# Kernel optimization log

Measured on AMD Instinct MI355X. Metric: run time of the kernel, lower is better.

The kernel has to match this reference:

```python
import jax, jax.numpy as jnp
import numpy as np

ALPHA = 0.2   # leaky_relu slope inside GAT/GCN
SLOPE = 0.01  # default F.leaky_relu slope in decoder MLPs


def _leaky(x, s):
    return jnp.where(x > 0, x, s * x)


def _gat(x, mask, W, a, b):
    # AttentionLayer.forward (eval mode: attention dropout off)
    h = x @ W                                   # [N, d]
    d = W.shape[1]
    e = _leaky(h @ a[:d] + (h @ a[d:]).T, ALPHA)  # dense [N, N] scores
    att = jax.nn.softmax(jnp.where(mask > 0, e, -9e15), axis=1)
    out = _leaky(att @ h, ALPHA)
    out = out / jnp.maximum(jnp.linalg.norm(out, axis=1, keepdims=True), 1e-12)  # F.normalize p=2 dim=1
    return out + b


def reference(x, adj, gcn_W, gcn_b, hgat_W, hgat_a, hgat_b, eta,
              l1_W, l1_a, l1_b, l2_W, l2_a, l2_b, l2_rW, l2_rb,
              tf1_W, tf1_b, tf2_W, tf2_b, tg1_W, tg1_b, tg2_W, tg2_b,
              mlp_W, mlp_b, train_sample):
    N = x.shape[0]
    # normalize_adj 'sym' via row/col scaling (avoids diag matmuls)
    rowsum = adj.sum(1)
    dis = rowsum ** -0.5
    dis = jnp.where(jnp.isinf(dis), 0.0, dis)
    gcn_adj = adj * dis[:, None] * dis[None, :]
    # normalize_adj(adj,'rw') is a no-op in the source -> gat_adj = adj + I
    gat_adj = adj + jnp.eye(N, dtype=adj.dtype)

    # HybridLayer (called with gcn_adj for both branches)
    gcn_out = _leaky(gcn_adj @ (x @ gcn_W + gcn_b), 0.2)
    gat_out = _gat(x, gcn_adj, hgat_W, hgat_a, hgat_b)
    h = eta * gcn_out + (1.0 - eta) * gat_out
    h = 0.7 * h + 0.3 * jax.lax.stop_gradient(h)  # x*0.7 + x.detach()*0.3
    h = jax.nn.selu(h)

    # ConvLayer1: ResAttention heads (in==out -> identity residual), mean reduce
    h1 = jnp.mean(jnp.stack([_gat(h, gat_adj, l1_W[i], l1_a[i], l1_b[i]) + h
                             for i in range(l1_W.shape[0])]), axis=0)
    h1 = jax.nn.selu(h1)

    # ConvLayer2: ResAttention heads with linear residual projection, mean reduce
    embed = jnp.mean(jnp.stack([_gat(h1, gat_adj, l2_W[i], l2_a[i], l2_b[i])
                                + (h1 @ l2_rW[i] + l2_rb[i])
                                for i in range(l2_W.shape[0])]), axis=0)

    # decoder MLPs (eval: p=0.01 dropout omitted for determinism)
    tf = _leaky(_leaky(embed @ tf1_W + tf1_b, SLOPE) @ tf2_W + tf2_b, SLOPE)
    tg = _leaky(_leaky(embed @ tg1_W + tg1_b, SLOPE) @ tg2_W + tg2_b, SLOPE)

    pair = jnp.concatenate([tf[train_sample[:, 0]], tg[train_sample[:, 1]]], axis=1)
    return pair @ mlp_W + mlp_b  # type='MLP' decode -> [B, 2]


def setup_inputs() -> dict:
    key = jax.random.key(0)
    ks = jax.random.split(key, 32)
    N, Din, H1, H2, H3, Dout, B, NH = 6144, 512, 256, 128, 64, 32, 4096, 2
    s = 0.05
    r = lambda k, sh: (jax.random.normal(k, sh, jnp.float32) * s)
    adj = (jax.random.uniform(ks[1], (N, N)) < 0.01).astype(jnp.float32)
    return {
        'x': jax.random.normal(ks[0], (N, Din), jnp.float32),
        'adj': adj,
        'gcn_W': r(ks[2], (Din, H1)), 'gcn_b': jnp.zeros((H1,), jnp.float32),
        'hgat_W': r(ks[3], (Din, H1)), 'hgat_a': r(ks[4], (2 * H1, 1)),
        'hgat_b': jnp.zeros((H1,), jnp.float32),
        'eta': jnp.array([0.5], jnp.float32),
        'l1_W': r(ks[5], (NH, H1, H1)), 'l1_a': r(ks[6], (NH, 2 * H1, 1)),
        'l1_b': jnp.zeros((NH, H1), jnp.float32),
        'l2_W': r(ks[7], (NH, H1, H2)), 'l2_a': r(ks[8], (NH, 2 * H2, 1)),
        'l2_b': jnp.zeros((NH, H2), jnp.float32),
        'l2_rW': r(ks[9], (NH, H1, H2)), 'l2_rb': jnp.zeros((NH, H2), jnp.float32),
        'tf1_W': r(ks[10], (H2, H3)), 'tf1_b': jnp.zeros((H3,), jnp.float32),
        'tf2_W': r(ks[11], (H3, Dout)), 'tf2_b': jnp.zeros((Dout,), jnp.float32),
        'tg1_W': r(ks[12], (H2, H3)), 'tg1_b': jnp.zeros((H3,), jnp.float32),
        'tg2_W': r(ks[13], (H3, Dout)), 'tg2_b': jnp.zeros((Dout,), jnp.float32),
        'mlp_W': r(ks[14], (2 * Dout, 2)), 'mlp_b': jnp.zeros((2,), jnp.float32),
        'train_sample': jax.random.randint(ks[15], (B, 2), 0, N, jnp.int32),
    }
```

## Files before the change

### kernel.cpp

```cpp
#include <hip/hip_runtime.h>
#include <math.h>


#define NN 6144
#define CAP 256

typedef __attribute__((ext_vector_type(8))) short bf16x8;
typedef __attribute__((ext_vector_type(4))) float f32x4;

__device__ __forceinline__ unsigned short f2bf(float v) {
  unsigned u = __float_as_uint(v);
  unsigned r = u + 0x7fffu + ((u >> 16) & 1u);
  return (unsigned short)(r >> 16);
}
__device__ __forceinline__ float bf2f(unsigned short h) {
  return __uint_as_float(((unsigned)h) << 16);
}
__device__ __forceinline__ float wave_max(float v) {
#pragma unroll
  for (int off = 32; off > 0; off >>= 1) v = fmaxf(v, __shfl_xor(v, off));
  return v;
}
__device__ __forceinline__ float wave_sum(float v) {
#pragma unroll
  for (int off = 32; off > 0; off >>= 1) v += __shfl_xor(v, off);
  return v;
}
__device__ __forceinline__ float selu_f(float x) {
  const float sc = 1.0507009873554805f, al = 1.6732632423543772f;
  return x > 0.0f ? sc * x : sc * al * (__expf(x) - 1.0f);
}
__device__ __forceinline__ void write_apack4(unsigned short* __restrict__ Ah,
    unsigned short* __restrict__ Al, int KC, int m, int k0,
    float v0, float v1, float v2, float v3) {
  int mt = m >> 4, c = k0 >> 5;
  int lane = ((k0 >> 3) & 3) * 16 + (m & 15);
  int j = k0 & 7;
  size_t base = ((size_t)(mt * KC + c) * 64 + lane) * 8 + j;
  ushort4 hi, lo;
  hi.x = f2bf(v0); lo.x = f2bf(v0 - bf2f(hi.x));
  hi.y = f2bf(v1); lo.y = f2bf(v1 - bf2f(hi.y));
  hi.z = f2bf(v2); lo.z = f2bf(v2 - bf2f(hi.z));
  hi.w = f2bf(v3); lo.w = f2bf(v3 - bf2f(hi.w));
  *(ushort4*)(Ah + base) = hi;
  *(ushort4*)(Al + base) = lo;
}

__global__ __launch_bounds__(256) void build_ell(const float* __restrict__ adj,
    unsigned short* __restrict__ nbr, int* __restrict__ deg,
    int* __restrict__ selfflag, float* __restrict__ dis)
{
  __shared__ unsigned long long mS[4][6][4];
  __shared__ int cntS[4];
  __shared__ int selfS;
  int i = blockIdx.x;
  int t = threadIdx.x, lane = t & 63, w = t >> 6;
  if (t == 0) selfS = 0;
  const float* row = adj + (size_t)i * NN + w * 1536;
  int cnt = 0;
  int hasself = 0;
#pragma unroll
  for (int it = 0; it < 6; ++it) {
    float4 v = *(const float4*)(row + it * 256 + lane * 4);
    unsigned long long m0 = __ballot(v.x != 0.0f);
    unsigned long long m1 = __ballot(v.y != 0.0f);
    unsigned long long m2 = __ballot(v.z != 0.0f);
    unsigned long long m3 = __ballot(v.w != 0.0f);
    if (lane == 0) {
      mS[w][it][0] = m0; mS[w][it][1] = m1; mS[w][it][2] = m2; mS[w][it][3] = m3;
    }
    cnt += __popcll(m0) + __popcll(m1) + __popcll(m2) + __popcll(m3);
  }
  if (lane == 0) cntS[w] = cnt;
  __syncthreads();
  int base = 0;
  for (int ww = 0; ww < w; ++ww) base += cntS[ww];
  unsigned long long below = (1ull << lane) - 1ull;
#pragma unroll
  for (int it = 0; it < 6; ++it) {
    unsigned long long m0 = mS[w][it][0], m1 = mS[w][it][1];
    unsigned long long m2 = mS[w][it][2], m3 = mS[w][it][3];
    int pre = __popcll(m0 & below) + __popcll(m1 & below) +
              __popcll(m2 & below) + __popcll(m3 & below);
    int c = w * 1536 + it * 256 + lane * 4;
    int p = base + pre;
    if ((m0 >> lane) & 1) { if (p < CAP) nbr[(size_t)i * CAP + p] = (unsigned short)c;     if (c == i) hasself = 1; p++; }
    if ((m1 >> lane) & 1) { if (p < CAP) nbr[(size_t)i * CAP + p] = (unsigned short)(c+1); if (c+1 == i) hasself = 1; p++; }
    if ((m2 >> lane) & 1) { if (p < CAP) nbr[(size_t)i * CAP + p] = (unsigned short)(c+2); if (c+2 == i) hasself = 1; p++; }
    if ((m3 >> lane) & 1) { if (p < CAP) nbr[(size_t)i * CAP + p] = (unsigned short)(c+3); if (c+3 == i) hasself = 1; }
    base += __popcll(m0) + __popcll(m1) + __popcll(m2) + __popcll(m3);
  }
  if (hasself) selfS = 1;
  __syncthreads();
  if (t == 0) {
    int total = cntS[0] + cntS[1] + cntS[2] + cntS[3];
    deg[i] = total < CAP ? total : CAP;
    selfflag[i] = selfS;
    dis[i] = (total > 0) ? rsqrtf((float)total) : 0.0f;
  }
}

__global__ __launch_bounds__(256) void pack_all(const float* __restrict__ gcn_W,
    const float* __restrict__ hgat_W, const float* __restrict__ l1_W,
    const float* __restrict__ l2_W, const float* __restrict__ l2_rW,
    const float* __restrict__ x,
    unsigned short* __restrict__ Bh, unsigned short* __restrict__ Bl,
    unsigned short* __restrict__ Ah, unsigned short* __restrict__ Al,
    float* __restrict__ fgZ)
{
  int idx = blockIdx.x * 256 + threadIdx.x;
  if (idx >= 520192) return;
  if (idx >= 458752) { fgZ[idx - 458752] = 0.0f; return; }
  if (idx >= 65536) {
    int rel = idx - 65536;
    int l = rel & 63;
    int mc = rel >> 6;
    int c = mc & 15, mt = mc >> 4;
    int m = mt * 16 + (l & 15);
    int kb = c * 32 + (l >> 4) * 8;
    const float* src = x + (size_t)m * 512 + kb;
    bf16x8 vh, vl;
#pragma unroll
    for (int j = 0; j < 8; ++j) {
      float v = src[j];
      unsigned short h = f2bf(v);
      vh[j] = (short)h;
      vl[j] = (short)f2bf(v - bf2f(h));
    }
    *(bf16x8*)(Ah + (size_t)rel * 8) = vh;
    *(bf16x8*)(Al + (size_t)rel * 8) = vl;
    return;
  }
  const float* B; int K, N, rel;
  if (idx < 32768) {
    B = (idx < 16384) ? gcn_W : hgat_W; K = 512; N = 256; rel = idx & 16383;
  } else if (idx < 49152) {
    B = (idx < 40960) ? l1_W : (l1_W + 65536); K = 256; N = 256; rel = (idx - 32768) & 8191;
  } else {
    int s = (idx - 49152) >> 12;
    B = (s == 0) ? l2_W : (s == 1) ? (l2_W + 32768) : (s == 2) ? l2_rW : (l2_rW + 32768);
    K = 256; N = 128; rel = (idx - 49152) & 4095;
  }
  int l = rel & 63;
  int tc = rel >> 6;
  int KC = K >> 5;
  int c = tc % KC, t = tc / KC;
  int n = t * 16 + (l & 15);
  int kb = c * 32 + (l >> 4) * 8;
  bf16x8 vh, vl;
#pragma unroll
  for (int j = 0; j < 8; ++j) {
    float v = B[(size_t)(kb + j) * N + n];
    unsigned short h = f2bf(v);
    vh[j] = (short)h;
    vl[j] = (short)f2bf(v - bf2f(h));
  }
  *(bf16x8*)(Bh + (size_t)idx * 8) = vh;
  *(bf16x8*)(Bl + (size_t)idx * 8) = vl;
}

__global__ __launch_bounds__(256) void gemm_mfma(
    const unsigned short* __restrict__ Ah, const unsigned short* __restrict__ Al,
    const unsigned short* __restrict__ Bh, const unsigned short* __restrict__ Bl,
    void* C0, void* C1, void* C2, void* C3,
    const float* b0, const float* b1, const float* b2, const float* b3,
    int KC, int N, long bStride8, int obf16mask,
    int fgmask, const float* __restrict__ aBase,
    float* __restrict__ fBase, float* __restrict__ gBase)
{
  int z = blockIdx.z;
  void* C = (z == 0) ? C0 : (z == 1) ? C1 : (z == 2) ? C2 : C3;
  const float* bias = (z == 0) ? b0 : (z == 1) ? b1 : (z == 2) ? b2 : b3;
  int obf = (obf16mask >> z) & 1;
  int wave = threadIdx.x >> 6, lane = threadIdx.x & 63;
  int mt = blockIdx.x * 4 + wave;
  int tg0 = blockIdx.y * 2;
  f32x4 acc[2];
  acc[0] = (f32x4){0.f, 0.f, 0.f, 0.f};
  acc[1] = (f32x4){0.f, 0.f, 0.f, 0.f};
  const bf16x8* ah = (const bf16x8*)Ah + (size_t)mt * KC * 64 + lane;
  const bf16x8* al = (const bf16x8*)Al + (size_t)mt * KC * 64 + lane;
  const bf16x8* bh = (const bf16x8*)Bh + (size_t)z * bStride8 + lane;
  const bf16x8* bl = (const bf16x8*)Bl + (size_t)z * bStride8 + lane;
  for (int c = 0; c < KC; ++c) {
    bf16x8 a_h = ah[c * 64];
    bf16x8 a_l = al[c * 64];
#pragma unroll
    for (int t = 0; t < 2; ++t) {
      size_t bo = (size_t)((tg0 + t) * KC + c) * 64;
      bf16x8 b_h = bh[bo];
      bf16x8 b_l = bl[bo];
      acc[t] = __builtin_amdgcn_mfma_f32_16x16x32_bf16(a_h, b_h, acc[t], 0, 0, 0);
      acc[t] = __builtin_amdgcn_mfma_f32_16x16x32_bf16(a_h, b_l, acc[t], 0, 0, 0);
      acc[t] = __builtin_amdgcn_mfma_f32_16x16x32_bf16(a_l, b_h, acc[t], 0, 0, 0);
    }
  }
  int quad = lane >> 4, cn = lane & 15;
#pragma unroll
  for (int t = 0; t < 2; ++t) {
    int col = (tg0 + t) * 16 + cn;
    float bv = bias ? bias[col] : 0.0f;
#pragma unroll
    for (int r = 0; r < 4; ++r) {
      int row = mt * 16 + quad * 4 + r;
      float v = acc[t][r] + bv;
      acc[t][r] = v;
      if (obf) ((unsigned short*)C)[(size_t)row * N + col] = f2bf(v);
      else     ((float*)C)[(size_t)row * N + col] = v;
    }
  }
  if ((fgmask >> z) & 1) {
    const float* af = aBase + (size_t)z * 2 * N;
    const float* ag = af + N;
    float af0 = af[tg0 * 16 + cn], af1 = af[(tg0 + 1) * 16 + cn];
    float ag0 = ag[tg0 * 16 + cn], ag1 = ag[(tg0 + 1) * 16 + cn];
#pragma unroll
    for (int r = 0; r < 4; ++r) {
      float pf = acc[0][r] * af0 + acc[1][r] * af1;
      float pg = acc[0][r] * ag0 + acc[1][r] * ag1;
#pragma unroll
      for (int off = 1; off < 16; off <<= 1) {
        pf += __shfl_xor(pf, off);
        pg += __shfl_xor(pg, off);
      }
      if (cn == 0) {
        int row = mt * 16 + quad * 4 + r;
        atomicAdd(fBase + (size_t)z * NN + row, pf);
        atomicAdd(gBase + (size_t)z * NN + row, pg);
      }
    }
  }
}

__device__ __forceinline__ void wave_softmax(const unsigned short* __restrict__ nbr,
    int row, int dg, int klen, float fi, const float* __restrict__ g,
    const float* __restrict__ dismask,
    int lane, int& j0, int& j1, float& a0, float& a1, float* dj0, float* dj1)
{
  float e0 = -3.0e38f, e1 = -3.0e38f;
  j0 = 0; j1 = 0;
  if (lane < klen) {
    j0 = (lane < dg) ? (int)nbr[(size_t)row * CAP + lane] : row;
    float ev = fi + g[j0];
    ev = ev > 0.0f ? ev : 0.2f * ev;
    if (dismask) {
      float dj = dismask[j0];
      if (dj0) *dj0 = dj;
      if (!(dj > 0.0f)) ev = -3.0e38f;
    }
    e0 = ev;
  }
  if (lane + 64 < klen) {
    j1 = (lane + 64 < dg) ? (int)nbr[(size_t)row * CAP + lane + 64] : row;
    float ev = fi + g[j1];
    ev = ev > 0.0f ? ev : 0.2f * ev;
    if (dismask) {
      float dj = dismask[j1];
      if (dj1) *dj1 = dj;
      if (!(dj > 0.0f)) ev = -3.0e38f;
    }
    e1 = ev;
  }
  float m = wave_max(fmaxf(e0, e1));
  float x0 = (lane < klen) ? __expf(e0 - m) : 0.0f;
  float x1 = (lane + 64 < klen) ? __expf(e1 - m) : 0.0f;
  float s = wave_sum(x0 + x1);
  float inv = 1.0f / s;
  a0 = x0 * inv;
  a1 = x1 * inv;
}

template<int D, int MODE>
__global__ __launch_bounds__(256) void gat_wave(const unsigned short* __restrict__ nbr,
    const int* __restrict__ deg, const int* __restrict__ selfflag,
    const float* __restrict__ f, const float* __restrict__ g,
    const unsigned short* __restrict__ hh, const float* __restrict__ bias,
    const float* __restrict__ res,
    unsigned short* __restrict__ Ah, unsigned short* __restrict__ Al,
    float* __restrict__ emb)
{
  __shared__ float attS[4][128];
  __shared__ unsigned short jS[4][128];
  __shared__ float xchg[2][2][D];
  int t = threadIdx.x, lane = t & 63, w = t >> 6;
  int r = w & 1, head = w >> 1;
  int row = blockIdx.x * 2 + r;
  const float* fh = f + (size_t)head * NN;
  const float* gh = g + (size_t)head * NN;
  const unsigned short* hhh = hh + (size_t)head * NN * D;
  int dg = deg[row];
  int klen = dg + (selfflag[row] ? 0 : 1);
  if (klen > 128) klen = 128;
  float fi = fh[row];
  int j0, j1; float a0, a1;
  wave_softmax(nbr, row, dg, klen, fi, gh, nullptr, lane, j0, j1, a0, a1,
               nullptr, nullptr);
  if (lane < klen)      { attS[w][lane] = a0;      jS[w][lane] = (unsigned short)j0; }
  if (lane + 64 < klen) { attS[w][lane + 64] = a1; jS[w][lane + 64] = (unsigned short)j1; }

  if (MODE == 1) {
    const unsigned short* hp = hhh + 4 * lane;
    float4 acc = {0.f, 0.f, 0.f, 0.f};
    for (int k = 0; k < klen; ++k) {
      float a = attS[w][k];
      ushort4 hv = *(const ushort4*)(hp + (size_t)jS[w][k] * D);
      acc.x += a * bf2f(hv.x);
      acc.y += a * bf2f(hv.y);
      acc.z += a * bf2f(hv.z);
      acc.w += a * bf2f(hv.w);
    }
    acc.x = acc.x > 0.f ? acc.x : 0.2f * acc.x;
    acc.y = acc.y > 0.f ? acc.y : 0.2f * acc.y;
    acc.z = acc.z > 0.f ? acc.z : 0.2f * acc.z;
    acc.w = acc.w > 0.f ? acc.w : 0.2f * acc.w;
    float q = wave_sum(acc.x * acc.x + acc.y * acc.y + acc.z * acc.z + acc.w * acc.w);
    float nsc = 1.0f / fmaxf(sqrtf(q), 1e-12f);
    const float* bh = bias + (size_t)head * D + 4 * lane;
    xchg[r][head][4 * lane]     = acc.x * nsc + bh[0];
    xchg[r][head][4 * lane + 1] = acc.y * nsc + bh[1];
    xchg[r][head][4 * lane + 2] = acc.z * nsc + bh[2];
    xchg[r][head][4 * lane + 3] = acc.w * nsc + bh[3];
    __syncthreads();
    if (head == 0) {
      int c = 4 * lane;
      float4 g0 = *(const float4*)&xchg[r][0][c];
      float4 g1 = *(const float4*)&xchg[r][1][c];
      float4 hv = *(const float4*)(res + (size_t)row * D + c);
      float o0 = selu_f(0.5f * (g0.x + g1.x) + hv.x);
      float o1 = selu_f(0.5f * (g0.y + g1.y) + hv.y);
      float o2 = selu_f(0.5f * (g0.z + g1.z) + hv.z);
      float o3 = selu_f(0.5f * (g0.w + g1.w) + hv.w);
      write_apack4(Ah, Al, 8, row, c, o0, o1, o2, o3);
    }
  } else {
    const unsigned short* hp = hhh + 2 * lane;
    float ax = 0.f, ay = 0.f;
    for (int k = 0; k < klen; ++k) {
      float a = attS[w][k];
      unsigned uv = *(const unsigned*)(hp + (size_t)jS[w][k] * D);
      ax += a * bf2f((unsigned short)(uv & 0xffffu));
      ay += a * bf2f((unsigned short)(uv >> 16));
    }
    ax = ax > 0.f ? ax : 0.2f * ax;
    ay = ay > 0.f ? ay : 0.2f * ay;
    float q = wave_sum(ax * ax + ay * ay);
    float nsc = 1.0f / fmaxf(sqrtf(q), 1e-12f);
    const float* bh = bias + (size_t)head * D + 2 * lane;
    xchg[r][head][2 * lane]     = ax * nsc + bh[0];
    xchg[r][head][2 * lane + 1] = ay * nsc + bh[1];
    __syncthreads();
    if (head == 0) {
      int c = 2 * lane;
      float g0a = xchg[r][0][c],     g1a = xchg[r][1][c];
      float g0b = xchg[r][0][c + 1], g1b = xchg[r][1][c + 1];
      const float* r0 = res + (size_t)row * D + c;
      const float* r1 = res + (size_t)NN * D + (size_t)row * D + c;
      float ea = 0.5f * ((g0a + r0[0]) + (g1a + r1[0]));
      float eb = 0.5f * ((g0b + r0[1]) + (g1b + r1[1]));
      emb[(size_t)row * D + c] = ea;
      emb[(size_t)row * D + c + 1] = eb;
    }
  }
}

__global__ __launch_bounds__(256) void fused_hybrid(const unsigned short* __restrict__ nbr,
    const int* __restrict__ deg, const float* __restrict__ dis,
    const unsigned short* __restrict__ xw, const unsigned short* __restrict__ hh,
    const float* __restrict__ f, const float* __restrict__ g,
    const float* __restrict__ bias, const float* __restrict__ eta,
    float* __restrict__ hout, unsigned short* __restrict__ Ah,
    unsigned short* __restrict__ Al)
{
  __shared__ float attS[4][128];
  __shared__ float djS[4][128];
  __shared__ unsigned short jS[4][128];
  int t = threadIdx.x, lane = t & 63, w = t >> 6;
  int row = blockIdx.x * 4 + w;
  int klen = deg[row];
  if (klen > 128) klen = 128;
  float fi = f[row];
  int j0, j1; float a0, a1; float d0 = 0.f, d1 = 0.f;
  wave_softmax(nbr, row, klen, klen, fi, g, dis, lane, j0, j1, a0, a1, &d0, &d1);
  if (lane < klen)      { attS[w][lane] = a0;      djS[w][lane] = d0;      jS[w][lane] = (unsigned short)j0; }
  if (lane + 64 < klen) { attS[w][lane + 64] = a1; djS[w][lane + 64] = d1; jS[w][lane + 64] = (unsigned short)j1; }

  const unsigned short* hp = hh + 4 * lane;
  const unsigned short* xp = xw + 4 * lane;
  float4 accA = {0.f, 0.f, 0.f, 0.f};
  float4 accG = {0.f, 0.f, 0.f, 0.f};
  for (int k = 0; k < klen; ++k) {
    float a = attS[w][k];
    float dj = djS[w][k];
    size_t jo = (size_t)jS[w][k] * 256;
    ushort4 hv = *(const ushort4*)(hp + jo);
    ushort4 xv = *(const ushort4*)(xp + jo);
    accA.x += a * bf2f(hv.x); accG.x += dj * bf2f(xv.x);
    accA.y += a * bf2f(hv.y); accG.y += dj * bf2f(xv.y);
    accA.z += a * bf2f(hv.z); accG.z += dj * bf2f(xv.z);
    accA.w += a * bf2f(hv.w); accG.w += dj * bf2f(xv.w);
  }
  accA.x = accA.x > 0.f ? accA.x : 0.2f * accA.x;
  accA.y = accA.y > 0.f ? accA.y : 0.2f * accA.y;
  accA.z = accA.z > 0.f ? accA.z : 0.2f * accA.z;
  accA.w = accA.w > 0.f ? accA.w : 0.2f * accA.w;
  float q = wave_sum(accA.x * accA.x + accA.y * accA.y +
                     accA.z * accA.z + accA.w * accA.w);
  float nsc = 1.0f / fmaxf(sqrtf(q), 1e-12f);
  float di = dis[row];
  float et = eta[0];
  const float* bp = bias + 4 * lane;
  float ga[4] = {accG.x, accG.y, accG.z, accG.w};
  float at[4] = {accA.x, accA.y, accA.z, accA.w};
  float hv4[4];
#pragma unroll
  for (int u = 0; u < 4; ++u) {
    float gcn = di * ga[u];
    gcn = gcn > 0.f ? gcn : 0.2f * gcn;
    float gat = at[u] * nsc + bp[u];
    float z = et * gcn + (1.0f - et) * gat;
    hv4[u] = selu_f(z);
  }
  *(float4*)(hout + (size_t)row * 256 + 4 * lane) =
      (float4){hv4[0], hv4[1], hv4[2], hv4[3]};
  write_apack4(Ah, Al, 8, row, 4 * lane, hv4[0], hv4[1], hv4[2], hv4[3]);
}

__global__ __launch_bounds__(256) void decoder_fused(const float* __restrict__ emb,
    const float* __restrict__ tf1_W, const float* __restrict__ tf1_b,
    const float* __restrict__ tf2_W, const float* __restrict__ tf2_b,
    const float* __restrict__ tg1_W, const float* __restrict__ tg1_b,
    const float* __restrict__ tg2_W, const float* __restrict__ tg2_b,
    float* __restrict__ TF, float* __restrict__ TG)
{
  __shared__ float embS[128 * 16];
  __shared__ float t1S[128 * 16];
  int t = threadIdx.x;
  int r0 = blockIdx.x * 16;
  for (int e = t; e < 2048; e += 256) {
    int r = e >> 7, k = e & 127;
    embS[k * 16 + r] = emb[(size_t)(r0 + r) * 128 + k];
  }
  __syncthreads();
  int c = t & 127, half = t >> 7;
  const float* W1 = (c < 64) ? tf1_W : tg1_W;
  int c1 = c & 63;
  float b1v = (c < 64) ? tf1_b[c1] : tg1_b[c1];
  float acc1[8];
#pragma unroll
  for (int r = 0; r < 8; ++r) acc1[r] = b1v;
  for (int k = 0; k < 128; ++k) {
    float wv = W1[k * 64 + c1];
#pragma unroll
    for (int r = 0; r < 8; ++r) acc1[r] += wv * embS[k * 16 + half * 8 + r];
  }
#pragma unroll
  for (int r = 0; r < 8; ++r) {
    float v = acc1[r];
    t1S[c * 16 + half * 8 + r] = v > 0.0f ? v : 0.01f * v;
  }
  __syncthreads();
  int c2 = t & 63, rg = t >> 6;
  const float* W2 = (c2 < 32) ? tf2_W : tg2_W;
  int cc = c2 & 31;
  float b2v = (c2 < 32) ? tf2_b[cc] : tg2_b[cc];
  int koff = (c2 < 32) ? 0 : 64;
  float acc2[4];
#pragma unroll
  for (int r = 0; r < 4; ++r) acc2[r] = b2v;
  for (int k = 0; k < 64; ++k) {
    float wv = W2[k * 32 + cc];
#pragma unroll
    for (int r = 0; r < 4; ++r) acc2[r] += wv * t1S[(koff + k) * 16 + rg * 4 + r];
  }
  float* O = (c2 < 32) ? TF : TG;
#pragma unroll
  for (int r = 0; r < 4; ++r) {
    float v = acc2[r];
    v = v > 0.0f ? v : 0.01f * v;
    O[(size_t)(r0 + rg * 4 + r) * 32 + cc] = v;
  }
}

__global__ void decode_mlp(const float* __restrict__ tf,
    const float* __restrict__ tg, const int* __restrict__ samp,
    const float* __restrict__ W, const float* __restrict__ b,
    float* __restrict__ out, int B)
{
  int bid = blockIdx.x * blockDim.x + threadIdx.x;
  if (bid >= B) return;
  int s0 = samp[2 * bid], s1 = samp[2 * bid + 1];
  float a0 = b[0], a1 = b[1];
#pragma unroll
  for (int c = 0; c < 32; ++c) {
    float v = tf[(size_t)s0 * 32 + c];
    a0 += v * W[2 * c];
    a1 += v * W[2 * c + 1];
  }
#pragma unroll
  for (int c = 0; c < 32; ++c) {
    float v = tg[(size_t)s1 * 32 + c];
    a0 += v * W[2 * (32 + c)];
    a1 += v * W[2 * (32 + c) + 1];
  }
  out[2 * bid] = a0;
  out[2 * bid + 1] = a1;
}

extern "C" void kernel_launch(void* const* d_in, const int* in_sizes, int n_in,
                              void* d_out, int out_size, void* d_ws, size_t ws_size,
                              hipStream_t stream)
{
  const float* x      = (const float*)d_in[0];
  const float* adj    = (const float*)d_in[1];
  const float* gcn_W  = (const float*)d_in[2];
  const float* gcn_b  = (const float*)d_in[3];
  const float* hgat_W = (const float*)d_in[4];
  const float* hgat_a = (const float*)d_in[5];
  const float* hgat_b = (const float*)d_in[6];
  const float* eta    = (const float*)d_in[7];
  const float* l1_W   = (const float*)d_in[8];
  const float* l1_a   = (const float*)d_in[9];
  const float* l1_b   = (const float*)d_in[10];
  const float* l2_W   = (const float*)d_in[11];
  const float* l2_a   = (const float*)d_in[12];
  const float* l2_b   = (const float*)d_in[13];
  const float* l2_rW  = (const float*)d_in[14];
  const float* l2_rb  = (const float*)d_in[15];
  const float* tf1_W  = (const float*)d_in[16];
  const float* tf1_b  = (const float*)d_in[17];
  const float* tf2_W  = (const float*)d_in[18];
  const float* tf2_b  = (const float*)d_in[19];
  const float* tg1_W  = (const float*)d_in[20];
  const float* tg1_b  = (const float*)d_in[21];
  const float* tg2_W  = (const float*)d_in[22];
  const float* tg2_b  = (const float*)d_in[23];
  const float* mlp_W  = (const float*)d_in[24];
  const float* mlp_b  = (const float*)d_in[25];
  const int*   samp   = (const int*)d_in[26];
  float* out = (float*)d_out;

  char* ws = (char*)d_ws;
  size_t off = 0;
  auto alloc = [&](size_t bytes) -> void* {
    void* p = ws + off;
    off += (bytes + 255) & ~(size_t)255;
    return p;
  };
  unsigned short* nbr = (unsigned short*)alloc((size_t)NN * CAP * 2);
  int*   deg = (int*)  alloc((size_t)NN * 4);
  int*   sfl = (int*)  alloc((size_t)NN * 4);
  float* dis = (float*)alloc((size_t)NN * 4);
  float* fgZ = (float*)alloc((size_t)10 * NN * 4);
  unsigned short* H0b = (unsigned short*)alloc((size_t)2 * NN * 256 * 2);
  float* Hh  = (float*)alloc((size_t)NN * 256 * 4);
  unsigned short* HHb = (unsigned short*)alloc((size_t)2 * NN * 256 * 2);
  unsigned short* Qb  = (unsigned short*)alloc((size_t)2 * NN * 128 * 2);
  float* Qr  = (float*)alloc((size_t)2 * NN * 128 * 4);
  float* emb = (float*)alloc((size_t)NN * 128 * 4);
  float* TF  = (float*)alloc((size_t)NN * 32 * 4);
  float* TG  = (float*)alloc((size_t)NN * 32 * 4);
  unsigned short* APH = (unsigned short*)alloc((size_t)NN * 512 * 2);
  unsigned short* APL = (unsigned short*)alloc((size_t)NN * 512 * 2);
  unsigned short* BPH = (unsigned short*)alloc((size_t)65536 * 8 * 2);
  unsigned short* BPL = (unsigned short*)alloc((size_t)65536 * 8 * 2);
  (void)ws_size; (void)n_in; (void)in_sizes; (void)out_size;

  float* fv0 = fgZ;
  float* gv0 = fgZ + NN;
  float* fv1 = fgZ + 2 * NN;
  float* gv1 = fgZ + 4 * NN;
  float* fv2 = fgZ + 6 * NN;
  float* gv2 = fgZ + 8 * NN;

  const float* nil = nullptr;

  build_ell<<<NN, 256, 0, stream>>>(adj, nbr, deg, sfl, dis);
  pack_all<<<2032, 256, 0, stream>>>(gcn_W, hgat_W, l1_W, l2_W, l2_rW, x,
      BPH, BPL, APH, APL, fgZ);

  gemm_mfma<<<dim3(96, 8, 2), 256, 0, stream>>>(APH, APL, BPH, BPL,
      H0b, H0b + (size_t)NN * 256, nullptr, nullptr, gcn_b, nil, nil, nil,
      16, 256, 16384, 0x3,
      0x2, hgat_a - 512, fv0 - NN, gv0 - NN);
  fused_hybrid<<<NN / 4, 256, 0, stream>>>(nbr, deg, dis, H0b, H0b + (size_t)NN * 256,
      fv0, gv0, hgat_b, eta, Hh, APH, APL);

  gemm_mfma<<<dim3(96, 8, 2), 256, 0, stream>>>(APH, APL, BPH + (size_t)32768 * 8,
      BPL + (size_t)32768 * 8, HHb, HHb + (size_t)NN * 256, nullptr, nullptr,
      nil, nil, nil, nil, 8, 256, 8192, 0x3,
      0x3, l1_a, fv1, gv1);
  gat_wave<256, 1><<<NN / 2, 256, 0, stream>>>(nbr, deg, sfl, fv1, gv1, HHb, l1_b,
      Hh, APH, APL, nullptr);

  gemm_mfma<<<dim3(96, 4, 4), 256, 0, stream>>>(APH, APL, BPH + (size_t)49152 * 8,
      BPL + (size_t)49152 * 8,
      Qb, Qb + (size_t)NN * 128, Qr, Qr + (size_t)NN * 128,
      nil, nil, l2_rb, l2_rb + 128, 8, 128, 4096, 0x3,
      0x3, l2_a, fv2, gv2);
  gat_wave<128, 2><<<NN / 2, 256, 0, stream>>>(nbr, deg, sfl, fv2, gv2, Qb, l2_b,
      Qr, nullptr, nullptr, emb);

  decoder_fused<<<NN / 16, 256, 0, stream>>>(emb, tf1_W, tf1_b, tf2_W, tf2_b,
      tg1_W, tg1_b, tg2_W, tg2_b, TF, TG);

  decode_mlp<<<16, 256, 0, stream>>>(TF, TG, samp, mlp_W, mlp_b, out, 4096);
}
```

Measured before the change: 427.3 us.

## Interleave head outputs so each wave gathers both heads per neighbor row

```diff
diff --git a/kernel.cpp b/kernel.cpp
--- a/kernel.cpp
+++ b/kernel.cpp
@@ -6,6 +6,7 @@
 #define CAP 256
 
 typedef __attribute__((ext_vector_type(8))) short bf16x8;
+typedef __attribute__((ext_vector_type(8))) unsigned short u16x8;
 typedef __attribute__((ext_vector_type(4))) float f32x4;
 
 __device__ __forceinline__ unsigned short f2bf(float v) {
@@ -30,6 +31,7 @@
   const float sc = 1.0507009873554805f, al = 1.6732632423543772f;
   return x > 0.0f ? sc * x : sc * al * (__expf(x) - 1.0f);
 }
+__device__ __forceinline__ float leaky2(float x) { return x > 0.f ? x : 0.2f * x; }
 __device__ __forceinline__ void write_apack4(unsigned short* __restrict__ Ah,
     unsigned short* __restrict__ Al, int KC, int m, int k0,
     float v0, float v1, float v2, float v3) {
@@ -164,14 +166,15 @@
     const unsigned short* __restrict__ Bh, const unsigned short* __restrict__ Bl,
     void* C0, void* C1, void* C2, void* C3,
     const float* b0, const float* b1, const float* b2, const float* b3,
-    int KC, int N, long bStride8, int obf16mask,
-    int fgmask, const float* __restrict__ aBase,
+    int KC, int N, long bStride8, int obf16mask, int ileaveG,
+    int fgmask, int fgIleave, const float* __restrict__ aBase,
     float* __restrict__ fBase, float* __restrict__ gBase)
 {
   int z = blockIdx.z;
   void* C = (z == 0) ? C0 : (z == 1) ? C1 : (z == 2) ? C2 : C3;
   const float* bias = (z == 0) ? b0 : (z == 1) ? b1 : (z == 2) ? b2 : b3;
   int obf = (obf16mask >> z) & 1;
+  int ilv = (ileaveG && z < 2) ? ileaveG : 0;
   int wave = threadIdx.x >> 6, lane = threadIdx.x & 63;
   int mt = blockIdx.x * 4 + wave;
   int tg0 = blockIdx.y * 2;
@@ -205,8 +208,15 @@
       int row = mt * 16 + quad * 4 + r;
       float v = acc[t][r] + bv;
       acc[t][r] = v;
-      if (obf) ((unsigned short*)C)[(size_t)row * N + col] = f2bf(v);
-      else     ((float*)C)[(size_t)row * N + col] = v;
+      if (ilv) {
+        size_t addr = (size_t)row * (2 * N) + (size_t)(col / ilv) * (2 * ilv)
+                    + z * ilv + (col % ilv);
+        ((unsigned short*)C0)[addr] = f2bf(v);
+      } else if (obf) {
+        ((unsigned short*)C)[(size_t)row * N + col] = f2bf(v);
+      } else {
+        ((float*)C)[(size_t)row * N + col] = v;
+      }
     }
   }
   if ((fgmask >> z) & 1) {
@@ -225,147 +235,114 @@
       }
       if (cn == 0) {
         int row = mt * 16 + quad * 4 + r;
-        atomicAdd(fBase + (size_t)z * NN + row, pf);
-        atomicAdd(gBase + (size_t)z * NN + row, pg);
+        size_t fo = fgIleave ? ((size_t)row * 2 + z) : ((size_t)z * NN + row);
+        atomicAdd(fBase + fo, pf);
+        atomicAdd(gBase + fo, pg);
       }
     }
   }
-}
-
-__device__ __forceinline__ void wave_softmax(const unsigned short* __restrict__ nbr,
-    int row, int dg, int klen, float fi, const float* __restrict__ g,
-    const float* __restrict__ dismask,
-    int lane, int& j0, int& j1, float& a0, float& a1, float* dj0, float* dj1)
-{
-  float e0 = -3.0e38f, e1 = -3.0e38f;
-  j0 = 0; j1 = 0;
-  if (lane < klen) {
-    j0 = (lane < dg) ? (int)nbr[(size_t)row * CAP + lane] : row;
-    float ev = fi + g[j0];
-    ev = ev > 0.0f ? ev : 0.2f * ev;
-    if (dismask) {
-      float dj = dismask[j0];
-      if (dj0) *dj0 = dj;
-      if (!(dj > 0.0f)) ev = -3.0e38f;
-    }
-    e0 = ev;
-  }
-  if (lane + 64 < klen) {
-    j1 = (lane + 64 < dg) ? (int)nbr[(size_t)row * CAP + lane + 64] : row;
-    float ev = fi + g[j1];
-    ev = ev > 0.0f ? ev : 0.2f * ev;
-    if (dismask) {
-      float dj = dismask[j1];
-      if (dj1) *dj1 = dj;
-      if (!(dj > 0.0f)) ev = -3.0e38f;
-    }
-    e1 = ev;
-  }
-  float m = wave_max(fmaxf(e0, e1));
-  float x0 = (lane < klen) ? __expf(e0 - m) : 0.0f;
-  float x1 = (lane + 64 < klen) ? __expf(e1 - m) : 0.0f;
-  float s = wave_sum(x0 + x1);
-  float inv = 1.0f / s;
-  a0 = x0 * inv;
-  a1 = x1 * inv;
 }
 
 template<int D, int MODE>
 __global__ __launch_bounds__(256) void gat_wave(const unsigned short* __restrict__ nbr,
     const int* __restrict__ deg, const int* __restrict__ selfflag,
-    const float* __restrict__ f, const float* __restrict__ g,
+    const float* __restrict__ fI, const float* __restrict__ gI,
     const unsigned short* __restrict__ hh, const float* __restrict__ bias,
     const float* __restrict__ res,
     unsigned short* __restrict__ Ah, unsigned short* __restrict__ Al,
     float* __restrict__ emb)
 {
-  __shared__ float attS[4][128];
+  __shared__ float2 attS[4][128];
   __shared__ unsigned short jS[4][128];
-  __shared__ float xchg[2][2][D];
   int t = threadIdx.x, lane = t & 63, w = t >> 6;
-  int r = w & 1, head = w >> 1;
-  int row = blockIdx.x * 2 + r;
-  const float* fh = f + (size_t)head * NN;
-  const float* gh = g + (size_t)head * NN;
-  const unsigned short* hhh = hh + (size_t)head * NN * D;
+  int row = blockIdx.x * 4 + w;
   int dg = deg[row];
   int klen = dg + (selfflag[row] ? 0 : 1);
   if (klen > 128) klen = 128;
-  float fi = fh[row];
-  int j0, j1; float a0, a1;
-  wave_softmax(nbr, row, dg, klen, fi, gh, nullptr, lane, j0, j1, a0, a1,
-               nullptr, nullptr);
-  if (lane < klen)      { attS[w][lane] = a0;      jS[w][lane] = (unsigned short)j0; }
-  if (lane + 64 < klen) { attS[w][lane + 64] = a1; jS[w][lane + 64] = (unsigned short)j1; }
+  float f0 = fI[2 * row], f1 = fI[2 * row + 1];
+  float e00 = -3.0e38f, e01 = -3.0e38f, e10 = -3.0e38f, e11 = -3.0e38f;
+  int j0 = 0, j1 = 0;
+  if (lane < klen) {
+    j0 = (lane < dg) ? (int)nbr[(size_t)row * CAP + lane] : row;
+    float2 gj = *(const float2*)(gI + 2 * j0);
+    e00 = leaky2(f0 + gj.x);
+    e01 = leaky2(f1 + gj.y);
+  }
+  if (lane + 64 < klen) {
+    j1 = (lane + 64 < dg) ? (int)nbr[(size_t)row * CAP + lane + 64] : row;
+    float2 gj = *(const float2*)(gI + 2 * j1);
+    e10 = leaky2(f0 + gj.x);
+    e11 = leaky2(f1 + gj.y);
+  }
+  float m0 = wave_max(fmaxf(e00, e10));
+  float m1 = wave_max(fmaxf(e01, e11));
+  float x00 = (lane < klen) ? __expf(e00 - m0) : 0.0f;
+  float x10 = (lane + 64 < klen) ? __expf(e10 - m0) : 0.0f;
+  float x01 = (lane < klen) ? __expf(e01 - m1) : 0.0f;
+  float x11 = (lane + 64 < klen) ? __expf(e11 - m1) : 0.0f;
+  float inv0 = 1.0f / wave_sum(x00 + x10);
+  float inv1 = 1.0f / wave_sum(x01 + x11);
+  if (lane < klen)      { attS[w][lane] = (float2){x00 * inv0, x01 * inv1};
+                          jS[w][lane] = (unsigned short)j0; }
+  if (lane + 64 < klen) { attS[w][lane + 64] = (float2){x10 * inv0, x11 * inv1};
+                          jS[w][lane + 64] = (unsigned short)j1; }
 
   if (MODE == 1) {
-    const unsigned short* hp = hhh + 4 * lane;
-    float4 acc = {0.f, 0.f, 0.f, 0.f};
+    const unsigned short* hp = hh + 8 * lane;
+    float4 a0 = {0.f, 0.f, 0.f, 0.f}, a1 = {0.f, 0.f, 0.f, 0.f};
     for (int k = 0; k < klen; ++k) {
-      float a = attS[w][k];
-      ushort4 hv = *(const ushort4*)(hp + (size_t)jS[w][k] * D);
-      acc.x += a * bf2f(hv.x);
-      acc.y += a * bf2f(hv.y);
-      acc.z += a * bf2f(hv.z);
-      acc.w += a * bf2f(hv.w);
-    }
-    acc.x = acc.x > 0.f ? acc.x : 0.2f * acc.x;
-    acc.y = acc.y > 0.f ? acc.y : 0.2f * acc.y;
-    acc.z = acc.z > 0.f ? acc.z : 0.2f * acc.z;
-    acc.w = acc.w > 0.f ? acc.w : 0.2f * acc.w;
-    float q = wave_sum(acc.x * acc.x + acc.y * acc.y + acc.z * acc.z + acc.w * acc.w);
-    float nsc = 1.0f / fmaxf(sqrtf(q), 1e-12f);
-    const float* bh = bias + (size_t)head * D + 4 * lane;
-    xchg[r][head][4 * lane]     = acc.x * nsc + bh[0];
-    xchg[r][head][4 * lane + 1] = acc.y * nsc + bh[1];
-    xchg[r][head][4 * lane + 2] = acc.z * nsc + bh[2];
-    xchg[r][head][4 * lane + 3] = acc.w * nsc + bh[3];
-    __syncthreads();
-    if (head == 0) {
-      int c = 4 * lane;
-      float4 g0 = *(const float4*)&xchg[r][0][c];
-      float4 g1 = *(const float4*)&xchg[r][1][c];
-      float4 hv = *(const float4*)(res + (size_t)row * D + c);
-      float o0 = selu_f(0.5f * (g0.x + g1.x) + hv.x);
-      float o1 = selu_f(0.5f * (g0.y + g1.y) + hv.y);
-      float o2 = selu_f(0.5f * (g0.z + g1.z) + hv.z);
-      float o3 = selu_f(0.5f * (g0.w + g1.w) + hv.w);
-      write_apack4(Ah, Al, 8, row, c, o0, o1, o2, o3);
-    }
+      float2 a = attS[w][k];
+      u16x8 hv = *(const u16x8*)(hp + (size_t)jS[w][k] * 512);
+      a0.x += a.x * bf2f(hv[0]); a1.x += a.y * bf2f(hv[4]);
+      a0.y += a.x * bf2f(hv[1]); a1.y += a.y * bf2f(hv[5]);
+      a0.z += a.x * bf2f(hv[2]); a1.z += a.y * bf2f(hv[6]);
+      a0.w += a.x * bf2f(hv[3]); a1.w += a.y * bf2f(hv[7]);
+    }
+    a0.x = leaky2(a0.x); a0.y = leaky2(a0.y); a0.z = leaky2(a0.z); a0.w = leaky2(a0.w);
+    a1.x = leaky2(a1.x); a1.y = leaky2(a1.y); a1.z = leaky2(a1.z); a1.w = leaky2(a1.w);
+    float q0 = wave_sum(a0.x * a0.x + a0.y * a0.y + a0.z * a0.z + a0.w * a0.w);
+    float q1 = wave_sum(a1.x * a1.x + a1.y * a1.y + a1.z * a1.z + a1.w * a1.w);
+    float n0 = 1.0f / fmaxf(sqrtf(q0), 1e-12f);
+    float n1 = 1.0f / fmaxf(sqrtf(q1), 1e-12f);
+    int c = 4 * lane;
+    float4 b0v = *(const float4*)(bias + c);
+    float4 b1v = *(const float4*)(bias + D + c);
+    float4 hv = *(const float4*)(res + (size_t)row * D + c);
+    float o0 = selu_f(0.5f * ((a0.x * n0 + b0v.x) + (a1.x * n1 + b1v.x)) + hv.x);
+    float o1 = selu_f(0.5f * ((a0.y * n0 + b0v.y) + (a1.y * n1 + b1v.y)) + hv.y);
+    float o2 = selu_f(0.5f * ((a0.z * n0 + b0v.z) + (a1.z * n1 + b1v.z)) + hv.z);
+    float o3 = selu_f(0.5f * ((a0.w * n0 + b0v.w) + (a1.w * n1 + b1v.w)) + hv.w);
+    write_apack4(Ah, Al, 8, row, c, o0, o1, o2, o3);
   } else {
-    const unsigned short* hp = hhh + 2 * lane;
-    float ax = 0.f, ay = 0.f;
+    const unsigned short* hp = hh + 4 * lane;
+    float a0x = 0.f, a0y = 0.f, a1x = 0.f, a1y = 0.f;
     for (int k = 0; k < klen; ++k) {
-      float a = attS[w][k];
-      unsigned uv = *(const unsigned*)(hp + (size_t)jS[w][k] * D);
-      ax += a * bf2f((unsigned short)(uv & 0xffffu));
-      ay += a * bf2f((unsigned short)(uv >> 16));
-    }
-    ax = ax > 0.f ? ax : 0.2f * ax;
-    ay = ay > 0.f ? ay : 0.2f * ay;
-    float q = wave_sum(ax * ax + ay * ay);
-    float nsc = 1.0f / fmaxf(sqrtf(q), 1e-12f);
-    const float* bh = bias + (size_t)head * D + 2 * lane;
-    xchg[r][head][2 * lane]     = ax * nsc + bh[0];
-    xchg[r][head][2 * lane + 1] = ay * nsc + bh[1];
-    __syncthreads();
-    if (head == 0) {
-      int c = 2 * lane;
-      float g0a = xchg[r][0][c],     g1a = xchg[r][1][c];
-      float g0b = xchg[r][0][c + 1], g1b = xchg[r][1][c + 1];
-      const float* r0 = res + (size_t)row * D + c;
-      const float* r1 = res + (size_t)NN * D + (size_t)row * D + c;
-      float ea = 0.5f * ((g0a + r0[0]) + (g1a + r1[0]));
-      float eb = 0.5f * ((g0b + r0[1]) + (g1b + r1[1]));
-      emb[(size_t)row * D + c] = ea;
-      emb[(size_t)row * D + c + 1] = eb;
-    }
+      float2 a = attS[w][k];
+      ushort4 hv = *(const ushort4*)(hp + (size_t)jS[w][k] * 256);
+      a0x += a.x * bf2f(hv.x); a0y += a.x * bf2f(hv.y);
+      a1x += a.y * bf2f(hv.z); a1y += a.y * bf2f(hv.w);
+    }
+    a0x = leaky2(a0x); a0y = leaky2(a0y);
+    a1x = leaky2(a1x); a1y = leaky2(a1y);
+    float q0 = wave_sum(a0x * a0x + a0y * a0y);
+    float q1 = wave_sum(a1x * a1x + a1y * a1y);
+    float n0 = 1.0f / fmaxf(sqrtf(q0), 1e-12f);
+    float n1 = 1.0f / fmaxf(sqrtf(q1), 1e-12f);
+    int c = 2 * lane;
+    float2 b0v = *(const float2*)(bias + c);
+    float2 b1v = *(const float2*)(bias + D + c);
+    float2 r0 = *(const float2*)(res + (size_t)row * D + c);
+    float2 r1 = *(const float2*)(res + (size_t)NN * D + (size_t)row * D + c);
+    float2 o;
+    o.x = 0.5f * (((a0x * n0 + b0v.x) + r0.x) + ((a1x * n1 + b1v.x) + r1.x));
+    o.y = 0.5f * (((a0y * n0 + b0v.y) + r0.y) + ((a1y * n1 + b1v.y) + r1.y));
+    *(float2*)(emb + (size_t)row * D + c) = o;
   }
 }
 
 __global__ __launch_bounds__(256) void fused_hybrid(const unsigned short* __restrict__ nbr,
     const int* __restrict__ deg, const float* __restrict__ dis,
-    const unsigned short* __restrict__ xw, const unsigned short* __restrict__ hh,
+    const unsigned short* __restrict__ XH,
     const float* __restrict__ f, const float* __restrict__ g,
     const float* __restrict__ bias, const float* __restrict__ eta,
     float* __restrict__ hout, unsigned short* __restrict__ Ah,
@@ -379,30 +356,44 @@
   int klen = deg[row];
   if (klen > 128) klen = 128;
   float fi = f[row];
-  int j0, j1; float a0, a1; float d0 = 0.f, d1 = 0.f;
-  wave_softmax(nbr, row, klen, klen, fi, g, dis, lane, j0, j1, a0, a1, &d0, &d1);
-  if (lane < klen)      { attS[w][lane] = a0;      djS[w][lane] = d0;      jS[w][lane] = (unsigned short)j0; }
-  if (lane + 64 < klen) { attS[w][lane + 64] = a1; djS[w][lane + 64] = d1; jS[w][lane + 64] = (unsigned short)j1; }
-
-  const unsigned short* hp = hh + 4 * lane;
-  const unsigned short* xp = xw + 4 * lane;
+  float e0 = -3.0e38f, e1 = -3.0e38f;
+  int j0 = 0, j1 = 0;
+  float d0 = 0.f, d1 = 0.f;
+  if (lane < klen) {
+    j0 = (int)nbr[(size_t)row * CAP + lane];
+    d0 = dis[j0];
+    float ev = leaky2(fi + g[j0]);
+    e0 = (d0 > 0.0f) ? ev : -3.0e38f;
+  }
+  if (lane + 64 < klen) {
+    j1 = (int)nbr[(size_t)row * CAP + lane + 64];
+    d1 = dis[j1];
+    float ev = leaky2(fi + g[j1]);
+    e1 = (d1 > 0.0f) ? ev : -3.0e38f;
+  }
+  float m = wave_max(fmaxf(e0, e1));
+  float x0 = (lane < klen) ? __expf(e0 - m) : 0.0f;
+  float x1 = (lane + 64 < klen) ? __expf(e1 - m) : 0.0f;
+  float inv = 1.0f / wave_sum(x0 + x1);
+  if (lane < klen)      { attS[w][lane] = x0 * inv;      djS[w][lane] = d0;
+                          jS[w][lane] = (unsigned short)j0; }
+  if (lane + 64 < klen) { attS[w][lane + 64] = x1 * inv; djS[w][lane + 64] = d1;
+                          jS[w][lane + 64] = (unsigned short)j1; }
+
+  const unsigned short* hp = XH + 8 * lane;
+  float4 accG = {0.f, 0.f, 0.f, 0.f};
   float4 accA = {0.f, 0.f, 0.f, 0.f};
-  float4 accG = {0.f, 0.f, 0.f, 0.f};
   for (int k = 0; k < klen; ++k) {
     float a = attS[w][k];
     float dj = djS[w][k];
-    size_t jo = (size_t)jS[w][k] * 256;
-    ushort4 hv = *(const ushort4*)(hp + jo);
-    ushort4 xv = *(const ushort4*)(xp + jo);
-    accA.x += a * bf2f(hv.x); accG.x += dj * bf2f(xv.x);
-    accA.y += a * bf2f(hv.y); accG.y += dj * bf2f(xv.y);
-    accA.z += a * bf2f(hv.z); accG.z += dj * bf2f(xv.z);
-    accA.w += a * bf2f(hv.w); accG.w += dj * bf2f(xv.w);
-  }
-  accA.x = accA.x > 0.f ? accA.x : 0.2f * accA.x;
-  accA.y = accA.y > 0.f ? accA.y : 0.2f * accA.y;
-  accA.z = accA.z > 0.f ? accA.z : 0.2f * accA.z;
-  accA.w = accA.w > 0.f ? accA.w : 0.2f * accA.w;
+    u16x8 hv = *(const u16x8*)(hp + (size_t)jS[w][k] * 512);
+    accG.x += dj * bf2f(hv[0]); accA.x += a * bf2f(hv[4]);
+    accG.y += dj * bf2f(hv[1]); accA.y += a * bf2f(hv[5]);
+    accG.z += dj * bf2f(hv[2]); accA.z += a * bf2f(hv[6]);
+    accG.w += dj * bf2f(hv[3]); accA.w += a * bf2f(hv[7]);
+  }
+  accA.x = leaky2(accA.x); accA.y = leaky2(accA.y);
+  accA.z = leaky2(accA.z); accA.w = leaky2(accA.w);
   float q = wave_sum(accA.x * accA.x + accA.y * accA.y +
                      accA.z * accA.z + accA.w * accA.w);
   float nsc = 1.0f / fmaxf(sqrtf(q), 1e-12f);
@@ -414,8 +405,7 @@
   float hv4[4];
 #pragma unroll
   for (int u = 0; u < 4; ++u) {
-    float gcn = di * ga[u];
-    gcn = gcn > 0.f ? gcn : 0.2f * gcn;
+    float gcn = leaky2(di * ga[u]);
     float gat = at[u] * nsc + bp[u];
     float z = et * gcn + (1.0f - et) * gat;
     hv4[u] = selu_f(z);
@@ -567,10 +557,10 @@
 
   float* fv0 = fgZ;
   float* gv0 = fgZ + NN;
-  float* fv1 = fgZ + 2 * NN;
-  float* gv1 = fgZ + 4 * NN;
-  float* fv2 = fgZ + 6 * NN;
-  float* gv2 = fgZ + 8 * NN;
+  float* fI1 = fgZ + 2 * NN;
+  float* gI1 = fgZ + 4 * NN;
+  float* fI2 = fgZ + 6 * NN;
+  float* gI2 = fgZ + 8 * NN;
 
   const float* nil = nullptr;
 
@@ -579,25 +569,25 @@
       BPH, BPL, APH, APL, fgZ);
 
   gemm_mfma<<<dim3(96, 8, 2), 256, 0, stream>>>(APH, APL, BPH, BPL,
-      H0b, H0b + (size_t)NN * 256, nullptr, nullptr, gcn_b, nil, nil, nil,
-      16, 256, 16384, 0x3,
-      0x2, hgat_a - 512, fv0 - NN, gv0 - NN);
-  fused_hybrid<<<NN / 4, 256, 0, stream>>>(nbr, deg, dis, H0b, H0b + (size_t)NN * 256,
+      H0b, nullptr, nullptr, nullptr, gcn_b, nil, nil, nil,
+      16, 256, 16384, 0x0, 4,
+      0x2, 0, hgat_a - 512, fv0 - NN, gv0 - NN);
+  fused_hybrid<<<NN / 4, 256, 0, stream>>>(nbr, deg, dis, H0b,
       fv0, gv0, hgat_b, eta, Hh, APH, APL);
 
   gemm_mfma<<<dim3(96, 8, 2), 256, 0, stream>>>(APH, APL, BPH + (size_t)32768 * 8,
-      BPL + (size_t)32768 * 8, HHb, HHb + (size_t)NN * 256, nullptr, nullptr,
-      nil, nil, nil, nil, 8, 256, 8192, 0x3,
-      0x3, l1_a, fv1, gv1);
-  gat_wave<256, 1><<<NN / 2, 256, 0, stream>>>(nbr, deg, sfl, fv1, gv1, HHb, l1_b,
+      BPL + (size_t)32768 * 8, HHb, nullptr, nullptr, nullptr,
+      nil, nil, nil, nil, 8, 256, 8192, 0x0, 4,
+      0x3, 1, l1_a, fI1, gI1);
+  gat_wave<256, 1><<<NN / 4, 256, 0, stream>>>(nbr, deg, sfl, fI1, gI1, HHb, l1_b,
       Hh, APH, APL, nullptr);
 
   gemm_mfma<<<dim3(96, 4, 4), 256, 0, stream>>>(APH, APL, BPH + (size_t)49152 * 8,
       BPL + (size_t)49152 * 8,
-      Qb, Qb + (size_t)NN * 128, Qr, Qr + (size_t)NN * 128,
-      nil, nil, l2_rb, l2_rb + 128, 8, 128, 4096, 0x3,
-      0x3, l2_a, fv2, gv2);
-  gat_wave<128, 2><<<NN / 2, 256, 0, stream>>>(nbr, deg, sfl, fv2, gv2, Qb, l2_b,
+      Qb, nullptr, Qr, Qr + (size_t)NN * 128,
+      nil, nil, l2_rb, l2_rb + 128, 8, 128, 4096, 0x0, 2,
+      0x3, 1, l2_a, fI2, gI2);
+  gat_wave<128, 2><<<NN / 4, 256, 0, stream>>>(nbr, deg, sfl, fI2, gI2, Qb, l2_b,
       Qr, nullptr, nullptr, emb);
 
   decoder_fused<<<NN / 16, 256, 0, stream>>>(emb, tf1_W, tf1_b, tf2_W, tf2_b,
```

Result: faster. 418.9 us (-2.0%).
